# Optimization experiments

Measured on AMD Instinct MI355X. Metric: run time of the kernel, lower is better.

The kernel has to match this reference:

```python
import jax, jax.numpy as jnp
import numpy as np
from jax import lax

T, B, C, N, NKV, H = 4, 8, 256, 2048, 2048, 8
EPS = 1e-5
TAU = 2.0
ALPHA = 4.0  # spikingjelly Sigmoid surrogate default
SCALE = 0.125

@jax.custom_vjp
def spike(x):
    return (x >= 0.0).astype(x.dtype)

def _spike_fwd(x):
    return (x >= 0.0).astype(x.dtype), x

def _spike_bwd(x, g):
    s = jax.nn.sigmoid(ALPHA * x)
    return (g * ALPHA * s * (1.0 - s),)

spike.defvjp(_spike_fwd, _spike_bwd)

def lif(x, v_th):
    # x: [T, ...]; multi-step LIF: v += (x - v)/tau, fire at v_th, hard reset to 0 (detach_reset)
    def step(v, xt):
        v = v + (xt - v) / TAU
        s = spike(v - v_th)
        v = v * (1.0 - lax.stop_gradient(s))
        return v, s
    _, s = lax.scan(step, jnp.zeros_like(x[0]), x)
    return s

def bn_apply(x, p):
    # x: [M, C, L]; p: [4, C] = (gamma, beta, running_mean, running_var); inference BN
    g, b, mu, var = p
    inv = g / jnp.sqrt(var + EPS)
    return (x - mu[:, None]) * inv[:, None] + b[:, None]

def repconv(x, w1, p1, w3, w2, p2):
    # x: [M, C, L] -> [M, C, L]
    x = jnp.einsum('oc,mcl->mol', w1, x)  # 1x1 conv
    g, b, mu, var = p1
    inv = g / jnp.sqrt(var + EPS)
    x = (x - mu[:, None]) * inv[:, None] + b[:, None]
    pad = b - mu * inv  # BNAndPadLayer pad values [C]
    pad = jnp.broadcast_to(pad[None, :, None], (x.shape[0], x.shape[1], 1))
    x = jnp.concatenate([pad, x, pad], axis=2)
    # depthwise conv k=3, valid
    x = x[:, :, :-2] * w3[:, 0:1] + x[:, :, 1:-1] * w3[:, 1:2] + x[:, :, 2:] * w3[:, 2:3]
    x = jnp.einsum('oc,mcl->mol', w2, x)  # 1x1 conv
    return bn_apply(x, p2)

def _make_bn(key, n):
    k1, k2, k3, k4 = jax.random.split(key, 4)
    g = jax.random.uniform(k1, (n, C)) * 0.5 + 0.75
    b = jax.random.normal(k2, (n, C)) * 0.1
    mu = jax.random.normal(k3, (n, C)) * 0.1
    var = jax.random.uniform(k4, (n, C)) + 0.5
    return jnp.stack([g, b, mu, var], axis=1).astype(jnp.float32)  # [n, 4, C]

def setup_inputs():
    key = jax.random.key(0)
    ks = jax.random.split(key, 8)
    q = jax.random.normal(ks[0], (T, B, C, N), dtype=jnp.float32)
    k_ = jax.random.normal(ks[1], (T, B, C, NKV), dtype=jnp.float32)
    s1 = 1.0 / np.sqrt(C).astype(np.float32)
    rc_w1 = jax.random.normal(ks[2], (6, C, C), dtype=jnp.float32) * s1
    rc_w3 = jax.random.normal(ks[3], (6, C, 3), dtype=jnp.float32) * 0.3
    rc_w2 = jax.random.normal(ks[4], (6, C, C), dtype=jnp.float32) * s1
    rc_bn1 = _make_bn(ks[5], 6)
    rc_bn2 = _make_bn(ks[6], 6)
    out_bn = _make_bn(ks[7], 6)
    return {"q": q, "k_": k_, "rc_w1": rc_w1, "rc_bn1": rc_bn1, "rc_w3": rc_w3,
            "rc_w2": rc_w2, "rc_bn2": rc_bn2, "out_bn": out_bn}

def reference(q, k_, rc_w1, rc_bn1, rc_w3, rc_w2, rc_bn2, out_bn):
    Tt, Bb, Cc, Nn = q.shape
    hd = Cc // H

    def conv_bn(x, i):  # RepConv(i) followed by BatchNorm1d(i), over flattened (T*B)
        L = x.shape[-1]
        y = x.reshape(Tt * Bb, Cc, L)
        y = repconv(y, rc_w1[i], rc_bn1[i], rc_w3[i], rc_w2[i], rc_bn2[i])
        y = bn_apply(y, out_bn[i])
        return y.reshape(Tt, Bb, Cc, L)

    qf = conv_bn(q, 0)
    kf = conv_bn(conv_bn(k_, 1), 2)
    vf = conv_bn(conv_bn(k_, 3), 4)

    def to_heads(x):  # [T,B,C,L] -> [T,B,H,L,hd]
        L = x.shape[-1]
        return x.transpose(0, 1, 3, 2).reshape(Tt, Bb, L, H, hd).transpose(0, 1, 3, 2, 4)

    qh = to_heads(lif(qf, 1.0))
    kh = to_heads(lif(kf, 1.0))
    vh = to_heads(lif(vf, 1.0))
    kv = jnp.einsum('tbhnd,tbhne->tbhde', kh, vh)          # [T,B,H,hd,hd]
    a = jnp.einsum('tbhmd,tbhde->tbhme', qh, kv) * SCALE   # [T,B,H,N,hd]
    a = a.transpose(0, 1, 2, 4, 3).reshape(Tt, Bb, Cc, Nn)
    a = lif(a, 0.5)  # attn_lif, v_threshold=0.5
    return conv_bn(a, 5)
```

## Files before the change

### kernel.cpp

```cpp
#include <hip/hip_runtime.h>

#define C 256
#define NPOS 2048
#define BB 8
#define TTIME 4
#define PRM_STRIDE 132096
#define FRAG_ELEMS 196608

typedef float f32x4 __attribute__((ext_vector_type(4)));
typedef short short8 __attribute__((ext_vector_type(8)));
typedef unsigned int u32x4 __attribute__((ext_vector_type(4)));

static __device__ __forceinline__ unsigned short f2bf(float f) {
    unsigned int u = __float_as_uint(f);
    return (unsigned short)((u + 0x7FFFu + ((u >> 16) & 1u)) >> 16);
}
static __device__ __forceinline__ float bf2f(unsigned short b) {
    return __uint_as_float(((unsigned int)b) << 16);
}
static __device__ __forceinline__ void split3(float f, unsigned short& h,
                                              unsigned short& m, unsigned short& l) {
    h = f2bf(f);
    float r1 = f - bf2f(h);
    m = f2bf(r1);
    float r2 = r1 - bf2f(m);
    l = f2bf(r2);
}
static __device__ __forceinline__ void tsplit_pair(float a, float b,
    unsigned int& hp, unsigned int& mp, unsigned int& lp) {
    unsigned int ua = __float_as_uint(a), ub = __float_as_uint(b);
    hp = (ua >> 16) | (ub & 0xFFFF0000u);
    float ra = a - __uint_as_float(ua & 0xFFFF0000u);
    float rb = b - __uint_as_float(ub & 0xFFFF0000u);
    unsigned int ura = __float_as_uint(ra), urb = __float_as_uint(rb);
    mp = (ura >> 16) | (urb & 0xFFFF0000u);
    float sa = ra - __uint_as_float(ura & 0xFFFF0000u);
    float sb = rb - __uint_as_float(urb & 0xFFFF0000u);
    lp = (__float_as_uint(sa) >> 16) | (__float_as_uint(sb) & 0xFFFF0000u);
}

__global__ __launch_bounds__(256) void prep_kern(
    const float* __restrict__ w1g, const float* __restrict__ bn1,
    const float* __restrict__ w3g, const float* __restrict__ w2g,
    const float* __restrict__ bn2, const float* __restrict__ bno,
    float* __restrict__ prm)
{
    int i = blockIdx.x;
    int tid = threadIdx.x;
    __shared__ float s1l[C], hcl[C], SGl[C];
    const float* b1 = bn1 + i * 4 * C;
    const float* b2 = bn2 + i * 4 * C;
    const float* bo = bno + i * 4 * C;
    float g1 = b1[tid], be1 = b1[C + tid], mu1 = b1[2 * C + tid], va1 = b1[3 * C + tid];
    float s1 = g1 / sqrtf(va1 + 1e-5f);
    float h1 = be1 - mu1 * s1;
    float g2 = b2[tid], be2 = b2[C + tid], mu2 = b2[2 * C + tid], va2 = b2[3 * C + tid];
    float s2 = g2 / sqrtf(va2 + 1e-5f);
    float h2 = be2 - mu2 * s2;
    float go = bo[tid], beo = bo[C + tid], muo = bo[2 * C + tid], vao = bo[3 * C + tid];
    float so = go / sqrtf(vao + 1e-5f);
    float ho = beo - muo * so;
    float SG = so * s2;
    float SH = so * h2 + ho;
    const float* w3i = w3g + i * C * 3;
    float w3s = w3i[tid * 3 + 0] + w3i[tid * 3 + 1] + w3i[tid * 3 + 2];
    s1l[tid] = s1; hcl[tid] = w3s * h1; SGl[tid] = SG;
    __syncthreads();
    float* prmi = prm + (size_t)i * PRM_STRIDE;
    const float* w1i = w1g + (size_t)i * C * C;
    const float* w2i = w2g + (size_t)i * C * C;
    for (int k = 0; k < C; ++k)
        prmi[tid * C + k] = s1l[k] * w1i[k * C + tid];
    for (int k = 0; k < C; ++k)
        prmi[65536 + tid * C + k] = SGl[k] * w2i[k * C + tid];
    for (int j = 0; j < 3; ++j)
        prmi[131072 + j * C + tid] = w3i[tid * 3 + j];
    float dot = 0.f;
    for (int k = 0; k < C; ++k)
        dot = fmaf(w2i[tid * C + k], hcl[k], dot);
    prmi[131840 + tid] = SG * dot + SH;
}

__global__ __launch_bounds__(256) void prep2_kern(
    const float* __restrict__ prm, unsigned short* __restrict__ frags)
{
    int b = blockIdx.x;
    int i = b >> 1, which = b & 1;
    const float* src = prm + (size_t)i * PRM_STRIDE + which * 65536;
    unsigned short* dst = frags + (size_t)b * FRAG_ELEMS;
    for (int e = threadIdx.x; e < 65536; e += 256) {
        int m = e & 255, k = e >> 8;
        float w = src[k * 256 + m];
        unsigned short h, mi, lo;
        split3(w, h, mi, lo);
        int ks = k >> 5, kin = k & 31;
        int mt = m >> 4;
        int lane = (m & 15) | (((kin >> 3) & 3) << 4);
        int j = kin & 7;
        size_t base = ((size_t)(ks * 16 + mt) * 3) * 64 * 8 + lane * 8 + j;
        dst[base] = h;
        dst[base + 512] = mi;
        dst[base + 1024] = lo;
    }
}

template<int IN_MODE, int OUT_T>
__global__ __launch_bounds__(256, 2) void conv_fused(
    const float* __restrict__ x, const unsigned int* __restrict__ xmask,
    float* __restrict__ y, const unsigned short* __restrict__ fragA,
    const unsigned short* __restrict__ fragB, const float* __restrict__ prmi)
{
    __shared__ __align__(16) char lds[30720];
    const int tid = threadIdx.x;
    const int lane = tid & 63, wv = tid >> 6;
    const int ctile = blockIdx.x & 31;
    const int slice = blockIdx.x >> 5;
    const int l0 = ctile * 64;
    const int lo4 = lane & 15, rg = lane >> 4;
    const int PA[6] = {0, 0, 1, 0, 2, 1};
    const int PB[6] = {0, 1, 0, 2, 0, 1};

    int mt[4];
#pragma unroll
    for (int rt = 0; rt < 4; ++rt) mt[rt] = wv + 4 * rt;

    f32x4 acc1[4][5];
#pragma unroll
    for (int a = 0; a < 4; ++a)
#pragma unroll
        for (int b = 0; b < 5; ++b) acc1[a][b] = (f32x4)0.f;

    const short8* Ab1 = (const short8*)fragA;

    float LDf[20];
    unsigned int LDu[20];

#define ISSUE(sp_)                                                             \
    {                                                                          \
        _Pragma("unroll")                                                      \
        for (int it = 0; it < 5; ++it) {                                       \
            int u = it * 256 + tid;                                            \
            int col = u % 80;                                                  \
            int kq4 = u / 80;                                                  \
            int gpos = l0 - 8 + col;                                           \
            bool ok = (unsigned)gpos < (unsigned)NPOS;                         \
            int k0 = (sp_) * 64 + kq4 * 4;                                     \
            if (IN_MODE == 2) {                                                \
                const unsigned int* mg = xmask + (size_t)slice * C * 64 + (gpos >> 5); \
                _Pragma("unroll")                                              \
                for (int j = 0; j < 4; ++j)                                    \
                    LDu[it * 4 + j] = ok ? mg[(k0 + j) * 64] : 0u;             \
            } else if (IN_MODE == 0) {                                         \
                const float* xg = x + (size_t)slice * C * NPOS + gpos;         \
                _Pragma("unroll")                                              \
                for (int j = 0; j < 4; ++j)                                    \
                    LDf[it * 4 + j] = ok ? xg[(size_t)(k0 + j) * NPOS] : 0.f;  \
            } else {                                                           \
                if (ok) {                                                      \
                    float4 a4 = *(const float4*)(x + ((size_t)slice * NPOS + gpos) * C + k0); \
                    LDf[it * 4 + 0] = a4.x; LDf[it * 4 + 1] = a4.y;            \
                    LDf[it * 4 + 2] = a4.z; LDf[it * 4 + 3] = a4.w;            \
                } else {                                                       \
                    _Pragma("unroll")                                          \
                    for (int j = 0; j < 4; ++j) LDf[it * 4 + j] = 0.f;         \
                }                                                              \
            }                                                                  \
        }                                                                      \
    }

#define SPLIT(sp_)                                                             \
    {                                                                          \
        _Pragma("unroll")                                                      \
        for (int it = 0; it < 5; ++it) {                                       \
            int u = it * 256 + tid;                                            \
            int col = u % 80;                                                  \
            int kq4 = u / 80;                                                  \
            int base = col * 128 + ((((kq4 >> 1) ^ (col & 7)) & 7) << 4) + (kq4 & 1) * 8; \
            if (IN_MODE == 2) {                                                \
                int gpos = l0 - 8 + col;                                       \
                int bitp = gpos & 31;                                          \
                unsigned int h01 = (((LDu[it * 4 + 0] >> bitp) & 1u) ? 0x3F80u : 0u)   \
                                 | (((LDu[it * 4 + 1] >> bitp) & 1u) ? 0x3F800000u : 0u); \
                unsigned int h23 = (((LDu[it * 4 + 2] >> bitp) & 1u) ? 0x3F80u : 0u)   \
                                 | (((LDu[it * 4 + 3] >> bitp) & 1u) ? 0x3F800000u : 0u); \
                *(unsigned long long*)(lds + base) =                           \
                    (unsigned long long)h01 | ((unsigned long long)h23 << 32); \
            } else {                                                           \
                unsigned int h01, m01, l01, h23, m23, l23;                     \
                tsplit_pair(LDf[it * 4 + 0], LDf[it * 4 + 1], h01, m01, l01);  \
                tsplit_pair(LDf[it * 4 + 2], LDf[it * 4 + 3], h23, m23, l23);  \
                *(unsigned long long*)(lds + base) =                           \
                    (unsigned long long)h01 | ((unsigned long long)h23 << 32); \
                *(unsigned long long*)(lds + 10240 + base) =                   \
                    (unsigned long long)m01 | ((unsigned long long)m23 << 32); \
                *(unsigned long long*)(lds + 20480 + base) =                   \
                    (unsigned long long)l01 | ((unsigned long long)l23 << 32); \
            }                                                                  \
        }                                                                      \
    }

    ISSUE(0);
#pragma unroll
    for (int sp = 0; sp < 4; ++sp) {
        SPLIT(sp);
        if (sp < 3) ISSUE(sp + 1);
        __syncthreads();
#pragma unroll
        for (int ksl = 0; ksl < 2; ++ksl) {
            int ks = sp * 2 + ksl;
            int oct = ksl * 4 + rg;
            short8 A[4][3];
#pragma unroll
            for (int rt = 0; rt < 4; ++rt)
#pragma unroll
                for (int s = 0; s < 3; ++s)
                    A[rt][s] = Ab1[(size_t)((ks * 16 + mt[rt]) * 3 + s) * 64 + lane];
            int ba[5];
#pragma unroll
            for (int ct = 0; ct < 5; ++ct) {
                int colb = ct * 16 + lo4;
                ba[ct] = colb * 128 + (((oct ^ (colb & 7)) & 7) << 4);
            }
            if (IN_MODE == 2) {
                short8 B[5];
#pragma unroll
                for (int ct = 0; ct < 5; ++ct)
                    B[ct] = *(const short8*)(lds + ba[ct]);
                __builtin_amdgcn_s_setprio(1);
#pragma unroll
                for (int pp = 0; pp < 3; ++pp)
#pragma unroll
                    for (int rt = 0; rt < 4; ++rt)
#pragma unroll
                        for (int ct = 0; ct < 5; ++ct)
                            acc1[rt][ct] = __builtin_amdgcn_mfma_f32_16x16x32_bf16(
                                A[rt][pp], B[ct], acc1[rt][ct], 0, 0, 0);
                __builtin_amdgcn_s_setprio(0);
            } else {
                short8 B[5][3];
#pragma unroll
                for (int ct = 0; ct < 5; ++ct) {
                    B[ct][0] = *(const short8*)(lds + ba[ct]);
                    B[ct][1] = *(const short8*)(lds + 10240 + ba[ct]);
                    B[ct][2] = *(const short8*)(lds + 20480 + ba[ct]);
                }
                __builtin_amdgcn_s_setprio(1);
#pragma unroll
                for (int pp = 0; pp < 6; ++pp)
#pragma unroll
                    for (int rt = 0; rt < 4; ++rt)
#pragma unroll
                        for (int ct = 0; ct < 5; ++ct)
                            acc1[rt][ct] = __builtin_amdgcn_mfma_f32_16x16x32_bf16(
                                A[rt][PA[pp]], B[ct][PB[pp]], acc1[rt][ct], 0, 0, 0);
                __builtin_amdgcn_s_setprio(0);
            }
        }
        __syncthreads();
    }

    const float* w3p = prmi + 131072;
    const short8* Ab2 = (const short8*)fragB;
    f32x4 acc2[4][4];
#pragma unroll
    for (int a = 0; a < 4; ++a)
#pragma unroll
        for (int b = 0; b < 4; ++b) acc2[a][b] = (f32x4)0.f;

#pragma unroll
    for (int s = 0; s < 4; ++s) {
        {
            const int rt = s;
            int RTB = mt[rt] << 4;
            float w3a[4], w3b[4], w3c[4];
#pragma unroll
            for (int r = 0; r < 4; ++r) {
                int m = RTB + rg * 4 + r;
                w3a[r] = w3p[m]; w3b[r] = w3p[256 + m]; w3c[r] = w3p[512 + m];
            }
            int k0 = (RTB & 63) + rg * 4;
#pragma unroll
            for (int ct = 0; ct < 5; ++ct) {
                int sc = ct * 16 + lo4;
                float tv[4];
#pragma unroll
                for (int r = 0; r < 4; ++r) {
                    float cur = acc1[rt][ct][r];
                    float prevv = acc1[rt][ct > 0 ? ct - 1 : 0][r];
                    float nextv = acc1[rt][ct < 4 ? ct + 1 : 4][r];
                    float sL  = __shfl(cur, lane - 1);
                    float sL2 = __shfl(prevv, lane + 15);
                    float sR  = __shfl(cur, lane + 1);
                    float sR2 = __shfl(nextv, lane - 15);
                    float uL = lo4 ? sL : sL2;
                    float uR = (lo4 == 15) ? sR2 : sR;
                    tv[r] = w3a[r] * uL + w3b[r] * cur + w3c[r] * uR;
                }
                if (sc >= 8 && sc < 72) {
                    int oc = sc - 8;
                    int base = oc * 128 + ((((k0 >> 3) ^ (oc & 7)) & 7) << 4) + (k0 & 7) * 2;
                    unsigned int h01, m01, l01, h23, m23, l23;
                    tsplit_pair(tv[0], tv[1], h01, m01, l01);
                    tsplit_pair(tv[2], tv[3], h23, m23, l23);
                    *(unsigned long long*)(lds + base) =
                        (unsigned long long)h01 | ((unsigned long long)h23 << 32);
                    *(unsigned long long*)(lds + 8192 + base) =
                        (unsigned long long)m01 | ((unsigned long long)m23 << 32);
                    *(unsigned long long*)(lds + 16384 + base) =
                        (unsigned long long)l01 | ((unsigned long long)l23 << 32);
                }
            }
        }
        __syncthreads();
#pragma unroll
        for (int ksl = 0; ksl < 2; ++ksl) {
            int ks = s * 2 + ksl;
            int chunk = ksl * 4 + rg;
            short8 A[4][3];
#pragma unroll
            for (int rt = 0; rt < 4; ++rt)
#pragma unroll
                for (int ss = 0; ss < 3; ++ss)
                    A[rt][ss] = Ab2[(size_t)((ks * 16 + mt[rt]) * 3 + ss) * 64 + lane];
            short8 B[4][3];
#pragma unroll
            for (int ct = 0; ct < 4; ++ct) {
                int oc = ct * 16 + lo4;
                int ba = oc * 128 + (((chunk ^ (oc & 7)) & 7) << 4);
                B[ct][0] = *(const short8*)(lds + ba);
                B[ct][1] = *(const short8*)(lds + 8192 + ba);
                B[ct][2] = *(const short8*)(lds + 16384 + ba);
            }
            __builtin_amdgcn_s_setprio(1);
#pragma unroll
            for (int pp = 0; pp < 6; ++pp)
#pragma unroll
                for (int rt = 0; rt < 4; ++rt)
#pragma unroll
                    for (int ct = 0; ct < 4; ++ct)
                        acc2[rt][ct] = __builtin_amdgcn_mfma_f32_16x16x32_bf16(
                            A[rt][PA[pp]], B[ct][PB[pp]], acc2[rt][ct], 0, 0, 0);
            __builtin_amdgcn_s_setprio(0);
        }
        __syncthreads();
    }

    const float* bs = prmi + 131840;
    float* yS = y + (size_t)slice * NPOS * C;
    if (OUT_T) {
#pragma unroll
        for (int ph = 0; ph < 4; ++ph) {
            if (ph) __syncthreads();
#pragma unroll
            for (int rt = 0; rt < 4; ++rt) {
                int m0 = (mt[rt] << 4) + rg * 4;
                int chunk = (mt[rt] << 2) + rg;
                int cl = lo4;
                f32x4 o;
#pragma unroll
                for (int r = 0; r < 4; ++r) o[r] = acc2[rt][ph][r] + bs[m0 + r];
                *(f32x4*)(lds + cl * 1024 + ((chunk ^ (cl & 7)) << 4)) = o;
            }
            __syncthreads();
#pragma unroll
            for (int i = 0; i < 4; ++i) {
                int u = i * 256 + tid;
                int cl = u >> 6, cchunk = u & 63;
                f32x4 o = *(const f32x4*)(lds + cl * 1024 + ((cchunk ^ (cl & 7)) << 4));
                int pos = l0 + ph * 16 + cl;
                *(f32x4*)(yS + (size_t)pos * C + cchunk * 4) = o;
            }
        }
    } else {
#pragma unroll
        for (int rt = 0; rt < 4; ++rt) {
            int m0 = (mt[rt] << 4) + rg * 4;
#pragma unroll
            for (int ct = 0; ct < 4; ++ct) {
                int pos = l0 + ct * 16 + lo4;
#pragma unroll
                for (int r = 0; r < 4; ++r)
                    yS[(size_t)(m0 + r) * NPOS + pos] = acc2[rt][ct][r] + bs[m0 + r];
            }
        }
    }
#undef ISSUE
#undef SPLIT
}

__global__ __launch_bounds__(256) void lif_kern(
    const float* __restrict__ yT, unsigned int* __restrict__ mask, float vth)
{
    int g = blockIdx.x * 256 + threadIdx.x;
    int ch = g & 255;
    int w = (g >> 8) & 63;
    int b = g >> 14;
    float v[32];
#pragma unroll
    for (int j = 0; j < 32; ++j) v[j] = 0.f;
    for (int t = 0; t < TTIME; ++t) {
        int slice = t * BB + b;
        const float* yr = yT + ((size_t)slice * NPOS + w * 32) * C + ch;
        unsigned int mw = 0;
#pragma unroll
        for (int j = 0; j < 32; ++j) {
            float yy = yr[(size_t)j * C];
            float vn = v[j] + (yy - v[j]) * 0.5f;
            int sp = (vn - vth) >= 0.0f;
            mw |= ((unsigned int)sp) << j;
            v[j] = sp ? 0.f : vn;
        }
        mask[((size_t)slice * C + ch) * 64 + w] = mw;
    }
}

__global__ __launch_bounds__(256) void kv_kern(
    const unsigned int* __restrict__ km_g, const unsigned int* __restrict__ vm_g,
    int* __restrict__ kv_g)
{
    int blk = blockIdx.x;
    int h = blk & 7;
    int tb = blk >> 3;
    __shared__ unsigned int km[32][65], vm[32][65];
    int tid = threadIdx.x;
#pragma unroll
    for (int i = 0; i < 8; ++i) {
        int idx = i * 256 + tid;
        int d = idx >> 6, w = idx & 63;
        size_t rb = ((size_t)tb * C + h * 32 + d) * 64 + w;
        km[d][w] = km_g[rb];
        vm[d][w] = vm_g[rb];
    }
    __syncthreads();
#pragma unroll
    for (int k = 0; k < 4; ++k) {
        int p = k * 256 + tid;
        int d = p >> 5, e = p & 31;
        int s = 0;
#pragma unroll
        for (int w = 0; w < 64; ++w)
            s += __popc(km[d][w] & vm[e][w]);
        kv_g[(size_t)blk * 1024 + p] = s;
    }
}

__global__ __launch_bounds__(256) void attn_kern(
    const unsigned int* __restrict__ qm_g, const int* __restrict__ kv_g,
    unsigned int* __restrict__ amask)
{
    int blk = blockIdx.x;
    int chunk = blk & 7;
    int bh = blk >> 3;
    int h = bh & 7, b = bh >> 3;
    int tid = threadIdx.x;
    __shared__ int kvs[1024];
    __shared__ unsigned int qw[32][8];
    float v[32];
#pragma unroll
    for (int e = 0; e < 32; ++e) v[e] = 0.f;
    for (int t = 0; t < TTIME; ++t) {
        int tb = t * BB + b;
        __syncthreads();
#pragma unroll
        for (int k = 0; k < 4; ++k)
            kvs[k * 256 + tid] = kv_g[((size_t)tb * 8 + h) * 1024 + k * 256 + tid];
        {
            int d = tid >> 3, wi = tid & 7;
            qw[d][wi] = qm_g[((size_t)tb * C + h * 32 + d) * 64 + chunk * 8 + wi];
        }
        __syncthreads();
        int a[32];
#pragma unroll
        for (int e = 0; e < 32; ++e) a[e] = 0;
        int wsel = tid >> 5, bitp = tid & 31;
        for (int d = 0; d < 32; ++d) {
            if ((qw[d][wsel] >> bitp) & 1u) {
                const int* kr = &kvs[d * 32];
#pragma unroll
                for (int e = 0; e < 32; ++e) a[e] += kr[e];
            }
        }
#pragma unroll
        for (int e = 0; e < 32; ++e) {
            float f = (float)a[e] * 0.125f;
            v[e] = v[e] + (f - v[e]) * 0.5f;
            int sp = (v[e] - 0.5f) >= 0.0f;
            unsigned long long bb = __ballot(sp);
            if ((tid & 63) == 0) {
                int ch = h * 32 + e;
                unsigned long long* dst = (unsigned long long*)amask
                    + ((size_t)tb * C + ch) * 32 + chunk * 4 + (tid >> 6);
                *dst = bb;
            }
            if (sp) v[e] = 0.f;
        }
    }
}

extern "C" void kernel_launch(void* const* d_in, const int* in_sizes, int n_in,
                              void* d_out, int out_size, void* d_ws, size_t ws_size,
                              hipStream_t stream) {
    const float* q   = (const float*)d_in[0];
    const float* k_  = (const float*)d_in[1];
    const float* w1g = (const float*)d_in[2];
    const float* bn1 = (const float*)d_in[3];
    const float* w3g = (const float*)d_in[4];
    const float* w2g = (const float*)d_in[5];
    const float* bn2 = (const float*)d_in[6];
    const float* bno = (const float*)d_in[7];

    float* prm = (float*)d_ws;
    unsigned short* frags = (unsigned short*)(prm + 6 * PRM_STRIDE);
    float* bufA = (float*)(frags + 12 * FRAG_ELEMS);
    float* bufB = bufA + 16777216;
    unsigned int* qmask = (unsigned int*)(bufB + 16777216);
    unsigned int* kmask = qmask + 524288;
    unsigned int* vmask = kmask + 524288;
    int* kvb = (int*)(vmask + 524288);
    unsigned int* amask = (unsigned int*)(kvb + 262144);

    prep_kern<<<6, 256, 0, stream>>>(w1g, bn1, w3g, w2g, bn2, bno, prm);
    prep2_kern<<<12, 256, 0, stream>>>(prm, frags);

#define FRAG(i, which) (frags + (size_t)((i) * 2 + (which)) * FRAG_ELEMS)
#define PRMI(i) (prm + (size_t)(i) * PRM_STRIDE)

    conv_fused<0, 1><<<1024, 256, 0, stream>>>(q, nullptr, bufA, FRAG(0, 0), FRAG(0, 1), PRMI(0));
    lif_kern<<<512, 256, 0, stream>>>(bufA, qmask, 1.0f);
    conv_fused<0, 1><<<1024, 256, 0, stream>>>(k_, nullptr, bufA, FRAG(1, 0), FRAG(1, 1), PRMI(1));
    conv_fused<1, 1><<<1024, 256, 0, stream>>>(bufA, nullptr, bufB, FRAG(2, 0), FRAG(2, 1), PRMI(2));
    lif_kern<<<512, 256, 0, stream>>>(bufB, kmask, 1.0f);
    conv_fused<0, 1><<<1024, 256, 0, stream>>>(k_, nullptr, bufA, FRAG(3, 0), FRAG(3, 1), PRMI(3));
    conv_fused<1, 1><<<1024, 256, 0, stream>>>(bufA, nullptr, bufB, FRAG(4, 0), FRAG(4, 1), PRMI(4));
    lif_kern<<<512, 256, 0, stream>>>(bufB, vmask, 1.0f);

    kv_kern<<<256, 256, 0, stream>>>(kmask, vmask, kvb);
    attn_kern<<<512, 256, 0, stream>>>(qmask, kvb, amask);

    conv_fused<2, 0><<<1024, 256, 0, stream>>>(nullptr, amask, (float*)d_out, FRAG(5, 0), FRAG(5, 1), PRMI(5));
}
```

Baseline: 794.2 us.

## Split conv_fused work across 16 waves with one row tile per wave

Raises the conv_fused block from 256 to 1024 threads so each of 16 waves owns a single 16-row output tile instead of four, shrinking the per-thread accumulator and fragment register arrays. The B-operand loads and MFMA loops are regrouped into smaller chunks, and the depthwise stage runs only in the waves owning the current 64-row slab. The intent is to cut register pressure and raise the number of resident waves for latency hiding. In exchange, each wave reloads the shared LDS B fragments, the depthwise step serialises across wave groups, and barriers now cover more waves.

```diff
diff --git a/kernel.cpp b/kernel.cpp
--- a/kernel.cpp
+++ b/kernel.cpp
@@ -105,7 +105,7 @@
 }
 
 template<int IN_MODE, int OUT_T>
-__global__ __launch_bounds__(256, 2) void conv_fused(
+__global__ __launch_bounds__(1024) void conv_fused(
     const float* __restrict__ x, const unsigned int* __restrict__ xmask,
     float* __restrict__ y, const unsigned short* __restrict__ fragA,
     const unsigned short* __restrict__ fragB, const float* __restrict__ prmi)
@@ -120,49 +120,45 @@
     const int PA[6] = {0, 0, 1, 0, 2, 1};
     const int PB[6] = {0, 1, 0, 2, 0, 1};
 
-    int mt[4];
-#pragma unroll
-    for (int rt = 0; rt < 4; ++rt) mt[rt] = wv + 4 * rt;
-
-    f32x4 acc1[4][5];
-#pragma unroll
-    for (int a = 0; a < 4; ++a)
-#pragma unroll
-        for (int b = 0; b < 5; ++b) acc1[a][b] = (f32x4)0.f;
+    f32x4 acc1[5];
+#pragma unroll
+    for (int b = 0; b < 5; ++b) acc1[b] = (f32x4)0.f;
 
     const short8* Ab1 = (const short8*)fragA;
 
-    float LDf[20];
-    unsigned int LDu[20];
+    float LDf[8];
+    unsigned int LDu[8];
 
 #define ISSUE(sp_)                                                             \
     {                                                                          \
         _Pragma("unroll")                                                      \
-        for (int it = 0; it < 5; ++it) {                                       \
-            int u = it * 256 + tid;                                            \
-            int col = u % 80;                                                  \
-            int kq4 = u / 80;                                                  \
-            int gpos = l0 - 8 + col;                                           \
-            bool ok = (unsigned)gpos < (unsigned)NPOS;                         \
-            int k0 = (sp_) * 64 + kq4 * 4;                                     \
-            if (IN_MODE == 2) {                                                \
-                const unsigned int* mg = xmask + (size_t)slice * C * 64 + (gpos >> 5); \
-                _Pragma("unroll")                                              \
-                for (int j = 0; j < 4; ++j)                                    \
-                    LDu[it * 4 + j] = ok ? mg[(k0 + j) * 64] : 0u;             \
-            } else if (IN_MODE == 0) {                                         \
-                const float* xg = x + (size_t)slice * C * NPOS + gpos;         \
-                _Pragma("unroll")                                              \
-                for (int j = 0; j < 4; ++j)                                    \
-                    LDf[it * 4 + j] = ok ? xg[(size_t)(k0 + j) * NPOS] : 0.f;  \
-            } else {                                                           \
-                if (ok) {                                                      \
-                    float4 a4 = *(const float4*)(x + ((size_t)slice * NPOS + gpos) * C + k0); \
-                    LDf[it * 4 + 0] = a4.x; LDf[it * 4 + 1] = a4.y;            \
-                    LDf[it * 4 + 2] = a4.z; LDf[it * 4 + 3] = a4.w;            \
+        for (int it = 0; it < 2; ++it) {                                       \
+            int u = it * 1024 + tid;                                           \
+            if (u < 1280) {                                                    \
+                int col = u % 80;                                              \
+                int kq4 = u / 80;                                              \
+                int gpos = l0 - 8 + col;                                       \
+                bool ok = (unsigned)gpos < (unsigned)NPOS;                     \
+                int k0 = (sp_) * 64 + kq4 * 4;                                 \
+                if (IN_MODE == 2) {                                            \
+                    const unsigned int* mg = xmask + (size_t)slice * C * 64 + (gpos >> 5); \
+                    _Pragma("unroll")                                          \
+                    for (int j = 0; j < 4; ++j)                                \
+                        LDu[it * 4 + j] = ok ? mg[(k0 + j) * 64] : 0u;         \
+                } else if (IN_MODE == 0) {                                     \
+                    const float* xg = x + (size_t)slice * C * NPOS + gpos;     \
+                    _Pragma("unroll")                                          \
+                    for (int j = 0; j < 4; ++j)                                \
+                        LDf[it * 4 + j] = ok ? xg[(size_t)(k0 + j) * NPOS] : 0.f; \
                 } else {                                                       \
-                    _Pragma("unroll")                                          \
-                    for (int j = 0; j < 4; ++j) LDf[it * 4 + j] = 0.f;         \
+                    if (ok) {                                                  \
+                        float4 a4 = *(const float4*)(x + ((size_t)slice * NPOS + gpos) * C + k0); \
+                        LDf[it * 4 + 0] = a4.x; LDf[it * 4 + 1] = a4.y;        \
+                        LDf[it * 4 + 2] = a4.z; LDf[it * 4 + 3] = a4.w;        \
+                    } else {                                                   \
+                        _Pragma("unroll")                                      \
+                        for (int j = 0; j < 4; ++j) LDf[it * 4 + j] = 0.f;     \
+                    }                                                          \
                 }                                                              \
             }                                                                  \
         }                                                                      \
@@ -171,30 +167,32 @@
 #define SPLIT(sp_)                                                             \
     {                                                                          \
         _Pragma("unroll")                                                      \
-        for (int it = 0; it < 5; ++it) {                                       \
-            int u = it * 256 + tid;                                            \
-            int col = u % 80;                                                  \
-            int kq4 = u / 80;                                                  \
-            int base = col * 128 + ((((kq4 >> 1) ^ (col & 7)) & 7) << 4) + (kq4 & 1) * 8; \
-            if (IN_MODE == 2) {                                                \
-                int gpos = l0 - 8 + col;                                       \
-                int bitp = gpos & 31;                                          \
-                unsigned int h01 = (((LDu[it * 4 + 0] >> bitp) & 1u) ? 0x3F80u : 0u)   \
-                                 | (((LDu[it * 4 + 1] >> bitp) & 1u) ? 0x3F800000u : 0u); \
-                unsigned int h23 = (((LDu[it * 4 + 2] >> bitp) & 1u) ? 0x3F80u : 0u)   \
-                                 | (((LDu[it * 4 + 3] >> bitp) & 1u) ? 0x3F800000u : 0u); \
-                *(unsigned long long*)(lds + base) =                           \
-                    (unsigned long long)h01 | ((unsigned long long)h23 << 32); \
-            } else {                                                           \
-                unsigned int h01, m01, l01, h23, m23, l23;                     \
-                tsplit_pair(LDf[it * 4 + 0], LDf[it * 4 + 1], h01, m01, l01);  \
-                tsplit_pair(LDf[it * 4 + 2], LDf[it * 4 + 3], h23, m23, l23);  \
-                *(unsigned long long*)(lds + base) =                           \
-                    (unsigned long long)h01 | ((unsigned long long)h23 << 32); \
-                *(unsigned long long*)(lds + 10240 + base) =                   \
-                    (unsigned long long)m01 | ((unsigned long long)m23 << 32); \
-                *(unsigned long long*)(lds + 20480 + base) =                   \
-                    (unsigned long long)l01 | ((unsigned long long)l23 << 32); \
+        for (int it = 0; it < 2; ++it) {                                       \
+            int u = it * 1024 + tid;                                           \
+            if (u < 1280) {                                                    \
+                int col = u % 80;                                              \
+                int kq4 = u / 80;                                              \
+                int base = col * 128 + ((((kq4 >> 1) ^ (col & 7)) & 7) << 4) + (kq4 & 1) * 8; \
+                if (IN_MODE == 2) {                                            \
+                    int gpos = l0 - 8 + col;                                   \
+                    int bitp = gpos & 31;                                      \
+                    unsigned int h01 = (((LDu[it * 4 + 0] >> bitp) & 1u) ? 0x3F80u : 0u)   \
+                                     | (((LDu[it * 4 + 1] >> bitp) & 1u) ? 0x3F800000u : 0u); \
+                    unsigned int h23 = (((LDu[it * 4 + 2] >> bitp) & 1u) ? 0x3F80u : 0u)   \
+                                     | (((LDu[it * 4 + 3] >> bitp) & 1u) ? 0x3F800000u : 0u); \
+                    *(unsigned long long*)(lds + base) =                       \
+                        (unsigned long long)h01 | ((unsigned long long)h23 << 32); \
+                } else {                                                       \
+                    unsigned int h01, m01, l01, h23, m23, l23;                 \
+                    tsplit_pair(LDf[it * 4 + 0], LDf[it * 4 + 1], h01, m01, l01); \
+                    tsplit_pair(LDf[it * 4 + 2], LDf[it * 4 + 3], h23, m23, l23); \
+                    *(unsigned long long*)(lds + base) =                       \
+                        (unsigned long long)h01 | ((unsigned long long)h23 << 32); \
+                    *(unsigned long long*)(lds + 10240 + base) =               \
+                        (unsigned long long)m01 | ((unsigned long long)m23 << 32); \
+                    *(unsigned long long*)(lds + 20480 + base) =               \
+                        (unsigned long long)l01 | ((unsigned long long)l23 << 32); \
+                }                                                              \
             }                                                                  \
         }                                                                      \
     }
@@ -209,12 +207,10 @@
         for (int ksl = 0; ksl < 2; ++ksl) {
             int ks = sp * 2 + ksl;
             int oct = ksl * 4 + rg;
-            short8 A[4][3];
-#pragma unroll
-            for (int rt = 0; rt < 4; ++rt)
-#pragma unroll
-                for (int s = 0; s < 3; ++s)
-                    A[rt][s] = Ab1[(size_t)((ks * 16 + mt[rt]) * 3 + s) * 64 + lane];
+            short8 A[3];
+#pragma unroll
+            for (int s = 0; s < 3; ++s)
+                A[s] = Ab1[(size_t)((ks * 16 + wv) * 3 + s) * 64 + lane];
             int ba[5];
 #pragma unroll
             for (int ct = 0; ct < 5; ++ct) {
@@ -230,30 +226,31 @@
 #pragma unroll
                 for (int pp = 0; pp < 3; ++pp)
 #pragma unroll
-                    for (int rt = 0; rt < 4; ++rt)
-#pragma unroll
-                        for (int ct = 0; ct < 5; ++ct)
-                            acc1[rt][ct] = __builtin_amdgcn_mfma_f32_16x16x32_bf16(
-                                A[rt][pp], B[ct], acc1[rt][ct], 0, 0, 0);
+                    for (int ct = 0; ct < 5; ++ct)
+                        acc1[ct] = __builtin_amdgcn_mfma_f32_16x16x32_bf16(
+                            A[pp], B[ct], acc1[ct], 0, 0, 0);
                 __builtin_amdgcn_s_setprio(0);
             } else {
-                short8 B[5][3];
-#pragma unroll
-                for (int ct = 0; ct < 5; ++ct) {
-                    B[ct][0] = *(const short8*)(lds + ba[ct]);
-                    B[ct][1] = *(const short8*)(lds + 10240 + ba[ct]);
-                    B[ct][2] = *(const short8*)(lds + 20480 + ba[ct]);
+#pragma unroll
+                for (int g = 0; g < 3; ++g) {
+                    const int nct = (g < 2) ? 2 : 1;
+                    const int c0g = g * 2;
+                    short8 B[2][3];
+#pragma unroll
+                    for (int cc = 0; cc < nct; ++cc) {
+                        B[cc][0] = *(const short8*)(lds + ba[c0g + cc]);
+                        B[cc][1] = *(const short8*)(lds + 10240 + ba[c0g + cc]);
+                        B[cc][2] = *(const short8*)(lds + 20480 + ba[c0g + cc]);
+                    }
+                    __builtin_amdgcn_s_setprio(1);
+#pragma unroll
+                    for (int pp = 0; pp < 6; ++pp)
+#pragma unroll
+                        for (int cc = 0; cc < nct; ++cc)
+                            acc1[c0g + cc] = __builtin_amdgcn_mfma_f32_16x16x32_bf16(
+                                A[PA[pp]], B[cc][PB[pp]], acc1[c0g + cc], 0, 0, 0);
+                    __builtin_amdgcn_s_setprio(0);
                 }
-                __builtin_amdgcn_s_setprio(1);
-#pragma unroll
-                for (int pp = 0; pp < 6; ++pp)
-#pragma unroll
-                    for (int rt = 0; rt < 4; ++rt)
-#pragma unroll
-                        for (int ct = 0; ct < 5; ++ct)
-                            acc1[rt][ct] = __builtin_amdgcn_mfma_f32_16x16x32_bf16(
-                                A[rt][PA[pp]], B[ct][PB[pp]], acc1[rt][ct], 0, 0, 0);
-                __builtin_amdgcn_s_setprio(0);
             }
         }
         __syncthreads();
@@ -261,33 +258,30 @@
 
     const float* w3p = prmi + 131072;
     const short8* Ab2 = (const short8*)fragB;
-    f32x4 acc2[4][4];
-#pragma unroll
-    for (int a = 0; a < 4; ++a)
-#pragma unroll
-        for (int b = 0; b < 4; ++b) acc2[a][b] = (f32x4)0.f;
+    f32x4 acc2[4];
+#pragma unroll
+    for (int b = 0; b < 4; ++b) acc2[b] = (f32x4)0.f;
 
 #pragma unroll
     for (int s = 0; s < 4; ++s) {
-        {
-            const int rt = s;
-            int RTB = mt[rt] << 4;
+        if ((wv >> 2) == s) {
+            int m0b = wv << 4;
             float w3a[4], w3b[4], w3c[4];
 #pragma unroll
             for (int r = 0; r < 4; ++r) {
-                int m = RTB + rg * 4 + r;
+                int m = m0b + rg * 4 + r;
                 w3a[r] = w3p[m]; w3b[r] = w3p[256 + m]; w3c[r] = w3p[512 + m];
             }
-            int k0 = (RTB & 63) + rg * 4;
+            int k0 = ((wv & 3) << 4) + rg * 4;
 #pragma unroll
             for (int ct = 0; ct < 5; ++ct) {
                 int sc = ct * 16 + lo4;
                 float tv[4];
 #pragma unroll
                 for (int r = 0; r < 4; ++r) {
-                    float cur = acc1[rt][ct][r];
-                    float prevv = acc1[rt][ct > 0 ? ct - 1 : 0][r];
-                    float nextv = acc1[rt][ct < 4 ? ct + 1 : 4][r];
+                    float cur = acc1[ct][r];
+                    float prevv = acc1[ct > 0 ? ct - 1 : 0][r];
+                    float nextv = acc1[ct < 4 ? ct + 1 : 4][r];
                     float sL  = __shfl(cur, lane - 1);
                     float sL2 = __shfl(prevv, lane + 15);
                     float sR  = __shfl(cur, lane + 1);
@@ -316,56 +310,53 @@
         for (int ksl = 0; ksl < 2; ++ksl) {
             int ks = s * 2 + ksl;
             int chunk = ksl * 4 + rg;
-            short8 A[4][3];
-#pragma unroll
-            for (int rt = 0; rt < 4; ++rt)
-#pragma unroll
-                for (int ss = 0; ss < 3; ++ss)
-                    A[rt][ss] = Ab2[(size_t)((ks * 16 + mt[rt]) * 3 + ss) * 64 + lane];
-            short8 B[4][3];
-#pragma unroll
-            for (int ct = 0; ct < 4; ++ct) {
-                int oc = ct * 16 + lo4;
-                int ba = oc * 128 + (((chunk ^ (oc & 7)) & 7) << 4);
-                B[ct][0] = *(const short8*)(lds + ba);
-                B[ct][1] = *(const short8*)(lds + 8192 + ba);
-                B[ct][2] = *(const short8*)(lds + 16384 + ba);
-            }
-            __builtin_amdgcn_s_setprio(1);
-#pragma unroll
-            for (int pp = 0; pp < 6; ++pp)
-#pragma unroll
-                for (int rt = 0; rt < 4; ++rt)
-#pragma unroll
-                    for (int ct = 0; ct < 4; ++ct)
-                        acc2[rt][ct] = __builtin_amdgcn_mfma_f32_16x16x32_bf16(
-                            A[rt][PA[pp]], B[ct][PB[pp]], acc2[rt][ct], 0, 0, 0);
-            __builtin_amdgcn_s_setprio(0);
+            short8 A[3];
+#pragma unroll
+            for (int ss = 0; ss < 3; ++ss)
+                A[ss] = Ab2[(size_t)((ks * 16 + wv) * 3 + ss) * 64 + lane];
+#pragma unroll
+            for (int g = 0; g < 2; ++g) {
+                const int c0g = g * 2;
+                short8 B[2][3];
+#pragma unroll
+                for (int cc = 0; cc < 2; ++cc) {
+                    int oc = (c0g + cc) * 16 + lo4;
+                    int ba = oc * 128 + (((chunk ^ (oc & 7)) & 7) << 4);
+                    B[cc][0] = *(const short8*)(lds + ba);
+                    B[cc][1] = *(const short8*)(lds + 8192 + ba);
+                    B[cc][2] = *(const short8*)(lds + 16384 + ba);
+                }
+                __builtin_amdgcn_s_setprio(1);
+#pragma unroll
+                for (int pp = 0; pp < 6; ++pp)
+#pragma unroll
+                    for (int cc = 0; cc < 2; ++cc)
+                        acc2[c0g + cc] = __builtin_amdgcn_mfma_f32_16x16x32_bf16(
+                            A[PA[pp]], B[cc][PB[pp]], acc2[c0g + cc], 0, 0, 0);
+                __builtin_amdgcn_s_setprio(0);
+            }
         }
         __syncthreads();
     }
 
     const float* bs = prmi + 131840;
     float* yS = y + (size_t)slice * NPOS * C;
+    const int m0 = (wv << 4) + rg * 4;
     if (OUT_T) {
+        const int chunk = (wv << 2) + rg;
 #pragma unroll
         for (int ph = 0; ph < 4; ++ph) {
             if (ph) __syncthreads();
-#pragma unroll
-            for (int rt = 0; rt < 4; ++rt) {
-                int m0 = (mt[rt] << 4) + rg * 4;
-                int chunk = (mt[rt] << 2) + rg;
+            {
                 int cl = lo4;
                 f32x4 o;
 #pragma unroll
-                for (int r = 0; r < 4; ++r) o[r] = acc2[rt][ph][r] + bs[m0 + r];
+                for (int r = 0; r < 4; ++r) o[r] = acc2[ph][r] + bs[m0 + r];
                 *(f32x4*)(lds + cl * 1024 + ((chunk ^ (cl & 7)) << 4)) = o;
             }
             __syncthreads();
-#pragma unroll
-            for (int i = 0; i < 4; ++i) {
-                int u = i * 256 + tid;
-                int cl = u >> 6, cchunk = u & 63;
+            {
+                int cl = tid >> 6, cchunk = tid & 63;
                 f32x4 o = *(const f32x4*)(lds + cl * 1024 + ((cchunk ^ (cl & 7)) << 4));
                 int pos = l0 + ph * 16 + cl;
                 *(f32x4*)(yS + (size_t)pos * C + cchunk * 4) = o;
@@ -373,15 +364,11 @@
         }
     } else {
 #pragma unroll
-        for (int rt = 0; rt < 4; ++rt) {
-            int m0 = (mt[rt] << 4) + rg * 4;
-#pragma unroll
-            for (int ct = 0; ct < 4; ++ct) {
-                int pos = l0 + ct * 16 + lo4;
-#pragma unroll
-                for (int r = 0; r < 4; ++r)
-                    yS[(size_t)(m0 + r) * NPOS + pos] = acc2[rt][ct][r] + bs[m0 + r];
-            }
+        for (int ct = 0; ct < 4; ++ct) {
+            int pos = l0 + ct * 16 + lo4;
+#pragma unroll
+            for (int r = 0; r < 4; ++r)
+                yS[(size_t)(m0 + r) * NPOS + pos] = acc2[ct][r] + bs[m0 + r];
         }
     }
 #undef ISSUE
@@ -525,17 +512,17 @@
 #define FRAG(i, which) (frags + (size_t)((i) * 2 + (which)) * FRAG_ELEMS)
 #define PRMI(i) (prm + (size_t)(i) * PRM_STRIDE)
 
-    conv_fused<0, 1><<<1024, 256, 0, stream>>>(q, nullptr, bufA, FRAG(0, 0), FRAG(0, 1), PRMI(0));
+    conv_fused<0, 1><<<1024, 1024, 0, stream>>>(q, nullptr, bufA, FRAG(0, 0), FRAG(0, 1), PRMI(0));
     lif_kern<<<512, 256, 0, stream>>>(bufA, qmask, 1.0f);
-    conv_fused<0, 1><<<1024, 256, 0, stream>>>(k_, nullptr, bufA, FRAG(1, 0), FRAG(1, 1), PRMI(1));
-    conv_fused<1, 1><<<1024, 256, 0, stream>>>(bufA, nullptr, bufB, FRAG(2, 0), FRAG(2, 1), PRMI(2));
+    conv_fused<0, 1><<<1024, 1024, 0, stream>>>(k_, nullptr, bufA, FRAG(1, 0), FRAG(1, 1), PRMI(1));
+    conv_fused<1, 1><<<1024, 1024, 0, stream>>>(bufA, nullptr, bufB, FRAG(2, 0), FRAG(2, 1), PRMI(2));
     lif_kern<<<512, 256, 0, stream>>>(bufB, kmask, 1.0f);
-    conv_fused<0, 1><<<1024, 256, 0, stream>>>(k_, nullptr, bufA, FRAG(3, 0), FRAG(3, 1), PRMI(3));
-    conv_fused<1, 1><<<1024, 256, 0, stream>>>(bufA, nullptr, bufB, FRAG(4, 0), FRAG(4, 1), PRMI(4));
+    conv_fused<0, 1><<<1024, 1024, 0, stream>>>(k_, nullptr, bufA, FRAG(3, 0), FRAG(3, 1), PRMI(3));
+    conv_fused<1, 1><<<1024, 1024, 0, stream>>>(bufA, nullptr, bufB, FRAG(4, 0), FRAG(4, 1), PRMI(4));
     lif_kern<<<512, 256, 0, stream>>>(bufB, vmask, 1.0f);
 
     kv_kern<<<256, 256, 0, stream>>>(kmask, vmask, kvb);
     attn_kern<<<512, 256, 0, stream>>>(qmask, kvb, amask);
 
-    conv_fused<2, 0><<<1024, 256, 0, stream>>>(nullptr, amask, (float*)d_out, FRAG(5, 0), FRAG(5, 1), PRMI(5));
-}
+    conv_fused<2, 0><<<1024, 1024, 0, stream>>>(nullptr, amask, (float*)d_out, FRAG(5, 0), FRAG(5, 1), PRMI(5));
+}
```

After: 907.1 us. 14.2% more time.

## Batch independent conv branches into multi-branch launches to fill the GPU

Applied to the files above, without the earlier changes.

Independent RepConv branches (q, k-stage1, v-stage1, then k-stage2 and v-stage2) are merged into single launches with 3072 or 2048 blocks, selected by the high bits of blockIdx. The LIF passes for k and v are merged into one kernel. The aim is to cut launch count and fill the device better than 1024-block grids, which may leave CUs idle at two blocks per CU. In exchange it needs extra workspace buffers, and falls back to the old sequence when the workspace is too small.

```diff
diff --git a/kernel.cpp b/kernel.cpp
--- a/kernel.cpp
+++ b/kernel.cpp
@@ -10,6 +10,15 @@
 typedef float f32x4 __attribute__((ext_vector_type(4)));
 typedef short short8 __attribute__((ext_vector_type(8)));
 typedef unsigned int u32x4 __attribute__((ext_vector_type(4)));
+
+struct CArgs {
+    const float* x;
+    const unsigned int* xmask;
+    float* y;
+    const unsigned short* fA;
+    const unsigned short* fB;
+    const float* prm;
+};
 
 static __device__ __forceinline__ unsigned short f2bf(float f) {
     unsigned int u = __float_as_uint(f);
@@ -104,17 +113,25 @@
     }
 }
 
-template<int IN_MODE, int OUT_T>
-__global__ __launch_bounds__(256, 2) void conv_fused(
-    const float* __restrict__ x, const unsigned int* __restrict__ xmask,
-    float* __restrict__ y, const unsigned short* __restrict__ fragA,
-    const unsigned short* __restrict__ fragB, const float* __restrict__ prmi)
+template<int IN_MODE, int OUT_T, int NB>
+__global__ __launch_bounds__(256, 2) void conv_fused(CArgs a0, CArgs a1, CArgs a2)
 {
     __shared__ __align__(16) char lds[30720];
     const int tid = threadIdx.x;
     const int lane = tid & 63, wv = tid >> 6;
     const int ctile = blockIdx.x & 31;
-    const int slice = blockIdx.x >> 5;
+    const int slice = (blockIdx.x >> 5) & 31;
+    const int branch = blockIdx.x >> 10;
+    CArgs a = a0;
+    if (NB > 1 && branch == 1) a = a1;
+    if (NB > 2 && branch == 2) a = a2;
+    const float* __restrict__ x = a.x;
+    const unsigned int* __restrict__ xmask = a.xmask;
+    float* __restrict__ y = a.y;
+    const unsigned short* __restrict__ fragA = a.fA;
+    const unsigned short* __restrict__ fragB = a.fB;
+    const float* __restrict__ prmi = a.prm;
+
     const int l0 = ctile * 64;
     const int lo4 = lane & 15, rg = lane >> 4;
     const int PA[6] = {0, 0, 1, 0, 2, 1};
@@ -126,9 +143,9 @@
 
     f32x4 acc1[4][5];
 #pragma unroll
-    for (int a = 0; a < 4; ++a)
-#pragma unroll
-        for (int b = 0; b < 5; ++b) acc1[a][b] = (f32x4)0.f;
+    for (int aa = 0; aa < 4; ++aa)
+#pragma unroll
+        for (int b = 0; b < 5; ++b) acc1[aa][b] = (f32x4)0.f;
 
     const short8* Ab1 = (const short8*)fragA;
 
@@ -263,9 +280,9 @@
     const short8* Ab2 = (const short8*)fragB;
     f32x4 acc2[4][4];
 #pragma unroll
-    for (int a = 0; a < 4; ++a)
-#pragma unroll
-        for (int b = 0; b < 4; ++b) acc2[a][b] = (f32x4)0.f;
+    for (int aa = 0; aa < 4; ++aa)
+#pragma unroll
+        for (int b = 0; b < 4; ++b) acc2[aa][b] = (f32x4)0.f;
 
 #pragma unroll
     for (int s = 0; s < 4; ++s) {
@@ -414,6 +431,36 @@
     }
 }
 
+__global__ __launch_bounds__(256) void lif2_kern(
+    const float* __restrict__ y0, unsigned int* __restrict__ m0,
+    const float* __restrict__ y1, unsigned int* __restrict__ m1, float vth)
+{
+    int which = blockIdx.x >> 9;
+    const float* yT = which ? y1 : y0;
+    unsigned int* mask = which ? m1 : m0;
+    int g = (blockIdx.x & 511) * 256 + threadIdx.x;
+    int ch = g & 255;
+    int w = (g >> 8) & 63;
+    int b = g >> 14;
+    float v[32];
+#pragma unroll
+    for (int j = 0; j < 32; ++j) v[j] = 0.f;
+    for (int t = 0; t < TTIME; ++t) {
+        int slice = t * BB + b;
+        const float* yr = yT + ((size_t)slice * NPOS + w * 32) * C + ch;
+        unsigned int mw = 0;
+#pragma unroll
+        for (int j = 0; j < 32; ++j) {
+            float yy = yr[(size_t)j * C];
+            float vn = v[j] + (yy - v[j]) * 0.5f;
+            int sp = (vn - vth) >= 0.0f;
+            mw |= ((unsigned int)sp) << j;
+            v[j] = sp ? 0.f : vn;
+        }
+        mask[((size_t)slice * C + ch) * 64 + w] = mw;
+    }
+}
+
 __global__ __launch_bounds__(256) void kv_kern(
     const unsigned int* __restrict__ km_g, const unsigned int* __restrict__ vm_g,
     int* __restrict__ kv_g)
@@ -518,24 +565,51 @@
     unsigned int* vmask = kmask + 524288;
     int* kvb = (int*)(vmask + 524288);
     unsigned int* amask = (unsigned int*)(kvb + 262144);
+    float* bufC = (float*)(amask + 524288);
+    float* bufD = bufC + 16777216;
+
+    const size_t BASE_BYTES  = (size_t)((char*)(amask + 524288) - (char*)d_ws);
+    const size_t NEED3 = BASE_BYTES + 67108864ull;
+    const size_t NEED4 = BASE_BYTES + 2ull * 67108864ull;
 
     prep_kern<<<6, 256, 0, stream>>>(w1g, bn1, w3g, w2g, bn2, bno, prm);
     prep2_kern<<<12, 256, 0, stream>>>(prm, frags);
 
 #define FRAG(i, which) (frags + (size_t)((i) * 2 + (which)) * FRAG_ELEMS)
 #define PRMI(i) (prm + (size_t)(i) * PRM_STRIDE)
-
-    conv_fused<0, 1><<<1024, 256, 0, stream>>>(q, nullptr, bufA, FRAG(0, 0), FRAG(0, 1), PRMI(0));
-    lif_kern<<<512, 256, 0, stream>>>(bufA, qmask, 1.0f);
-    conv_fused<0, 1><<<1024, 256, 0, stream>>>(k_, nullptr, bufA, FRAG(1, 0), FRAG(1, 1), PRMI(1));
-    conv_fused<1, 1><<<1024, 256, 0, stream>>>(bufA, nullptr, bufB, FRAG(2, 0), FRAG(2, 1), PRMI(2));
-    lif_kern<<<512, 256, 0, stream>>>(bufB, kmask, 1.0f);
-    conv_fused<0, 1><<<1024, 256, 0, stream>>>(k_, nullptr, bufA, FRAG(3, 0), FRAG(3, 1), PRMI(3));
-    conv_fused<1, 1><<<1024, 256, 0, stream>>>(bufA, nullptr, bufB, FRAG(4, 0), FRAG(4, 1), PRMI(4));
-    lif_kern<<<512, 256, 0, stream>>>(bufB, vmask, 1.0f);
+#define CA(xx, mm, yy, ii) CArgs{ (xx), (mm), (yy), FRAG(ii, 0), FRAG(ii, 1), PRMI(ii) }
+
+    CArgs nil = CA((const float*)nullptr, (const unsigned int*)nullptr, (float*)nullptr, 0);
+
+    if (ws_size >= NEED4) {
+        conv_fused<0, 1, 3><<<3072, 256, 0, stream>>>(
+            CA(q, nullptr, bufA, 0), CA(k_, nullptr, bufB, 1), CA(k_, nullptr, bufC, 3));
+        lif_kern<<<512, 256, 0, stream>>>(bufA, qmask, 1.0f);
+        conv_fused<1, 1, 2><<<2048, 256, 0, stream>>>(
+            CA(bufB, nullptr, bufA, 2), CA(bufC, nullptr, bufD, 4), nil);
+        lif2_kern<<<1024, 256, 0, stream>>>(bufA, kmask, bufD, vmask, 1.0f);
+    } else if (ws_size >= NEED3) {
+        conv_fused<0, 1, 3><<<3072, 256, 0, stream>>>(
+            CA(q, nullptr, bufA, 0), CA(k_, nullptr, bufB, 1), CA(k_, nullptr, bufC, 3));
+        lif_kern<<<512, 256, 0, stream>>>(bufA, qmask, 1.0f);
+        conv_fused<1, 1, 1><<<1024, 256, 0, stream>>>(CA(bufB, nullptr, bufA, 2), nil, nil);
+        lif_kern<<<512, 256, 0, stream>>>(bufA, kmask, 1.0f);
+        conv_fused<1, 1, 1><<<1024, 256, 0, stream>>>(CA(bufC, nullptr, bufA, 4), nil, nil);
+        lif_kern<<<512, 256, 0, stream>>>(bufA, vmask, 1.0f);
+    } else {
+        conv_fused<0, 1, 1><<<1024, 256, 0, stream>>>(CA(q, nullptr, bufA, 0), nil, nil);
+        lif_kern<<<512, 256, 0, stream>>>(bufA, qmask, 1.0f);
+        conv_fused<0, 1, 1><<<1024, 256, 0, stream>>>(CA(k_, nullptr, bufA, 1), nil, nil);
+        conv_fused<1, 1, 1><<<1024, 256, 0, stream>>>(CA(bufA, nullptr, bufB, 2), nil, nil);
+        lif_kern<<<512, 256, 0, stream>>>(bufB, kmask, 1.0f);
+        conv_fused<0, 1, 1><<<1024, 256, 0, stream>>>(CA(k_, nullptr, bufA, 3), nil, nil);
+        conv_fused<1, 1, 1><<<1024, 256, 0, stream>>>(CA(bufA, nullptr, bufB, 4), nil, nil);
+        lif_kern<<<512, 256, 0, stream>>>(bufB, vmask, 1.0f);
+    }
 
     kv_kern<<<256, 256, 0, stream>>>(kmask, vmask, kvb);
     attn_kern<<<512, 256, 0, stream>>>(qmask, kvb, amask);
 
-    conv_fused<2, 0><<<1024, 256, 0, stream>>>(nullptr, amask, (float*)d_out, FRAG(5, 0), FRAG(5, 1), PRMI(5));
-}
+    conv_fused<2, 0, 1><<<1024, 256, 0, stream>>>(
+        CArgs{ nullptr, amask, (float*)d_out, FRAG(5, 0), FRAG(5, 1), PRMI(5) }, nil, nil);
+}
```

New measurement: 802.3 us. Within noise of the previous version (+1.0%).
